# Kernel tuning notes

Measured on AMD Instinct MI355X. Metric: run time of the kernel, lower is better.

## Reference

```python
import jax, jax.numpy as jnp
import numpy as np

B, S, D = 2, 2048, 2048
H, G = 16, 4
HD = D // H          # head_dim = 128
KV = HD * G          # 512


def setup_inputs() -> dict:
    key = jax.random.key(0)
    ks = jax.random.split(key, 5)
    scale = 1.0 / np.sqrt(D)
    return {
        "x": jax.random.normal(ks[0], (B, S, D), dtype=jnp.float32),
        "Wqkv": jax.random.normal(ks[1], (D, D + 2 * KV), dtype=jnp.float32) * scale,
        "bqkv": jax.random.normal(ks[2], (D + 2 * KV,), dtype=jnp.float32) * 0.01,
        "Wout": jax.random.normal(ks[3], (D, D), dtype=jnp.float32) * scale,
        "bout": jax.random.normal(ks[4], (D,), dtype=jnp.float32) * 0.01,
    }


def reference(x, Wqkv, bqkv, Wout, bout):
    b, s, _ = x.shape
    qkv = x @ Wqkv + bqkv                                  # [b, s, D + 2*KV]
    q, k, v = jnp.split(qkv, [D, D + KV], axis=-1)
    q = q.reshape(b, s, H, HD)                             # [b, s, H, hd]
    # torch .repeat tiles the group axis: head h -> group (h % G)
    k = jnp.tile(k.reshape(b, s, G, HD), (1, 1, H // G, 1))  # [b, s, H, hd]
    v = jnp.tile(v.reshape(b, s, G, HD), (1, 1, H // G, 1))
    # NOTE: original divides by head_dim (not sqrt(head_dim)) -- kept faithfully
    scores = jnp.einsum("bqhd,bkhd->bhqk", q, k) / HD      # [b, H, s, s]
    prob = jax.nn.softmax(scores, axis=-1)
    out = jnp.einsum("bhqk,bkhd->bqhd", prob, v).reshape(b, s, D)
    return out @ Wout + bout
```

## Files before the change

### kernel.cpp

```cpp
#include <hip/hip_runtime.h>
#include <stdint.h>

typedef __bf16 bf16;
typedef __bf16 bf16x8 __attribute__((ext_vector_type(8)));
typedef __bf16 bf16x4 __attribute__((ext_vector_type(4)));
typedef float  f32x4  __attribute__((ext_vector_type(4)));

#define B_   2
#define S_   2048
#define D_   2048
#define H_   16
#define G_   4
#define HD_  128
#define KV_  512
#define NQKV 3072
#define M_   4096

__device__ __forceinline__ void async16(bf16* lds, const bf16* g) {
  __builtin_amdgcn_global_load_lds(
      (const __attribute__((address_space(1))) unsigned int*)g,
      (__attribute__((address_space(3))) unsigned int*)lds, 16, 0, 0);
}

__device__ __forceinline__ f32x4 mfma16(bf16x8 a, bf16x8 b, f32x4 c) {
  return __builtin_amdgcn_mfma_f32_16x16x32_bf16(a, b, c, 0, 0, 0);
}

__global__ void convert_x_kernel(const float* __restrict__ in,
                                 bf16* __restrict__ out, int n4) {
  int i = blockIdx.x * blockDim.x + threadIdx.x;
  if (i >= n4) return;
  float4 v = ((const float4*)in)[i];
  bf16x4 o = { (bf16)v.x, (bf16)v.y, (bf16)v.z, (bf16)v.w };
  *(bf16x4*)(out + (size_t)i * 4) = o;
}

__global__ void transpose_w_kernel(const float* __restrict__ in,
                                   bf16* __restrict__ out,
                                   int rows, int cols) {
  __shared__ float tile[32][33];
  int bc = blockIdx.x * 32;
  int br = blockIdx.y * 32;
  int tx = threadIdx.x, ty = threadIdx.y;
  #pragma unroll
  for (int i = 0; i < 32; i += 8)
    tile[ty + i][tx] = in[(size_t)(br + ty + i) * cols + bc + tx];
  __syncthreads();
  #pragma unroll
  for (int i = 0; i < 32; i += 8)
    out[(size_t)(bc + ty + i) * rows + br + tx] = (bf16)tile[tx][ty + i];
}

__global__ void transpose_v_kernel(const bf16* __restrict__ qkv,
                                   bf16* __restrict__ vt) {
  __shared__ bf16 tile[32][33];
  int bg = blockIdx.z; int b = bg / G_, g = bg % G_;
  int sb = blockIdx.x * 32, db = blockIdx.y * 32;
  int tx = threadIdx.x, ty = threadIdx.y;
  const bf16* src = qkv + (size_t)b * S_ * NQKV + (D_ + KV_ + g * HD_);
  #pragma unroll
  for (int i = 0; i < 32; i += 8)
    tile[ty + i][tx] = src[(size_t)(sb + ty + i) * NQKV + db + tx];
  __syncthreads();
  bf16* dst = vt + (size_t)(b * G_ + g) * HD_ * S_;
  #pragma unroll
  for (int i = 0; i < 32; i += 8)
    dst[(size_t)(db + ty + i) * S_ + sb + tx] = tile[tx][ty + i];
}

template <int OUT_BF16>
__global__ __launch_bounds__(256) void gemm_bt(const bf16* __restrict__ A,
                                               const bf16* __restrict__ Bt,
                                               const float* __restrict__ bias,
                                               void* __restrict__ Cout,
                                               int Ndim, int K) {
  __shared__ __align__(16) bf16 As[128 * 32];
  __shared__ __align__(16) bf16 Bs[128 * 32];
  int t = threadIdx.x;
  int w = t >> 6, l = t & 63, lr = l & 15, lg = l >> 4;
  int wm = w >> 1, wn = w & 1;
  int row0 = blockIdx.x * 128, col0 = blockIdx.y * 128;

  f32x4 acc[4][4] = {};

  const bf16* ga = A  + (size_t)(row0 + (t >> 2)) * K + (t & 3) * 8;
  const bf16* gb = Bt + (size_t)(col0 + (t >> 2)) * K + (t & 3) * 8;

  for (int k0 = 0; k0 < K; k0 += 32) {
    __syncthreads();
    #pragma unroll
    for (int i = 0; i < 2; i++)
      async16(&As[w * 512 + i * 2048], ga + (size_t)i * 64 * K + k0);
    #pragma unroll
    for (int i = 0; i < 2; i++)
      async16(&Bs[w * 512 + i * 2048], gb + (size_t)i * 64 * K + k0);
    __syncthreads();

    bf16x8 af[4], bfr[4];
    #pragma unroll
    for (int mi = 0; mi < 4; mi++)
      af[mi] = *(const bf16x8*)&As[(wm * 64 + mi * 16 + lr) * 32 + lg * 8];
    #pragma unroll
    for (int ni = 0; ni < 4; ni++)
      bfr[ni] = *(const bf16x8*)&Bs[(wn * 64 + ni * 16 + lr) * 32 + lg * 8];
    #pragma unroll
    for (int mi = 0; mi < 4; mi++)
      #pragma unroll
      for (int ni = 0; ni < 4; ni++)
        acc[mi][ni] = mfma16(af[mi], bfr[ni], acc[mi][ni]);
  }

  float bv[4];
  #pragma unroll
  for (int ni = 0; ni < 4; ni++)
    bv[ni] = bias[col0 + wn * 64 + ni * 16 + lr];

  #pragma unroll
  for (int mi = 0; mi < 4; mi++)
    #pragma unroll
    for (int ni = 0; ni < 4; ni++)
      #pragma unroll
      for (int r = 0; r < 4; r++) {
        int row = row0 + wm * 64 + mi * 16 + lg * 4 + r;
        int col = col0 + wn * 64 + ni * 16 + lr;
        float v = acc[mi][ni][r] + bv[ni];
        if (OUT_BF16)
          ((bf16*)Cout)[(size_t)row * Ndim + col] = (bf16)v;
        else
          ((float*)Cout)[(size_t)row * Ndim + col] = v;
      }
}

__global__ __launch_bounds__(256, 2) void attn_kernel(const bf16* __restrict__ qkv,
                                                      const bf16* __restrict__ vt,
                                                      bf16* __restrict__ attnb) {
  __shared__ __align__(16) bf16 Ks[64 * 128];
  __shared__ __align__(16) bf16 Vs[128 * 64];
  __shared__ __align__(16) bf16 Ps[4][32 * 64];

  int t = threadIdx.x, w = t >> 6, l = t & 63, lr = l & 15, lg = l >> 4;
  int rsw = lr & 7;
  int bh = blockIdx.y, b = bh >> 4, h = bh & 15, g = h & 3;
  int q0 = blockIdx.x * 128;

  bf16x8 qf[2][4];
  #pragma unroll
  for (int mi = 0; mi < 2; mi++) {
    const bf16* qbase = qkv + (size_t)(b * S_ + q0 + w * 32 + mi * 16 + lr) * NQKV + h * HD_;
    #pragma unroll
    for (int kc = 0; kc < 4; kc++)
      qf[mi][kc] = *(const bf16x8*)(qbase + kc * 32 + lg * 8);
  }

  const bf16* kbase = qkv + (size_t)b * S_ * NQKV + D_ + g * HD_;
  const bf16* vbase = vt + (size_t)(b * G_ + g) * HD_ * S_;

  int krowi = w * 4 + (l >> 4);
  int ksw = (l & 15) ^ (krowi & 7);
  const bf16* kgl = kbase + (size_t)krowi * NQKV + ksw * 8;
  int vrowi = w * 8 + (l >> 3);
  int vsw = (l & 7) ^ ((l >> 3) & 7);
  const bf16* vgl = vbase + (size_t)vrowi * S_ + vsw * 8;

  float lsum[2][4] = {};
  f32x4 accO[2][8] = {};

  for (int kv0 = 0; kv0 < S_; kv0 += 64) {
    __syncthreads();
    #pragma unroll
    for (int i = 0; i < 4; i++)
      async16(&Ks[w * 512 + i * 2048], kgl + (size_t)(kv0 + i * 16) * NQKV);
    #pragma unroll
    for (int i = 0; i < 4; i++)
      async16(&Vs[w * 512 + i * 2048], vgl + (size_t)(i * 32) * S_ + kv0);
    __syncthreads();

    f32x4 sacc[2][4] = {};
    __builtin_amdgcn_s_setprio(1);
    #pragma unroll
    for (int fk = 0; fk < 4; fk++) {
      bf16x8 kf[4];
      #pragma unroll
      for (int kc = 0; kc < 4; kc++)
        kf[kc] = *(const bf16x8*)&Ks[(fk * 16 + lr) * 128 + (((kc * 4 + lg) ^ rsw) * 8)];
      #pragma unroll
      for (int mi = 0; mi < 2; mi++)
        #pragma unroll
        for (int kc = 0; kc < 4; kc++)
          sacc[mi][fk] = mfma16(qf[mi][kc], kf[kc], sacc[mi][fk]);
    }
    __builtin_amdgcn_s_setprio(0);

    bf16* psw = &Ps[w][0];
    #pragma unroll
    for (int mi = 0; mi < 2; mi++)
      #pragma unroll
      for (int fk = 0; fk < 4; fk++)
        #pragma unroll
        for (int r = 0; r < 4; r++) {
          float pv = __expf(sacc[mi][fk][r] * 0.0078125f);
          lsum[mi][r] += pv;
          int prow = mi * 16 + lg * 4 + r;
          psw[prow * 64 + (((fk * 2 + (lr >> 3)) ^ (prow & 7)) * 8) + (lr & 7)] = (bf16)pv;
        }

    bf16x8 pa[2][2];
    #pragma unroll
    for (int mi = 0; mi < 2; mi++)
      #pragma unroll
      for (int kk = 0; kk < 2; kk++)
        pa[mi][kk] = *(const bf16x8*)&psw[(mi * 16 + lr) * 64 + (((kk * 4 + lg) ^ rsw) * 8)];

    __builtin_amdgcn_s_setprio(1);
    #pragma unroll
    for (int fd = 0; fd < 8; fd++) {
      bf16x8 vfr[2];
      #pragma unroll
      for (int kk = 0; kk < 2; kk++)
        vfr[kk] = *(const bf16x8*)&Vs[(fd * 16 + lr) * 64 + (((kk * 4 + lg) ^ rsw) * 8)];
      #pragma unroll
      for (int mi = 0; mi < 2; mi++)
        #pragma unroll
        for (int kk = 0; kk < 2; kk++)
          accO[mi][fd] = mfma16(pa[mi][kk], vfr[kk], accO[mi][fd]);
    }
    __builtin_amdgcn_s_setprio(0);
  }

  #pragma unroll
  for (int mi = 0; mi < 2; mi++)
    #pragma unroll
    for (int r = 0; r < 4; r++) {
      float s = lsum[mi][r];
      #pragma unroll
      for (int o = 1; o < 16; o <<= 1) s += __shfl_xor(s, o);
      lsum[mi][r] = 1.f / s;
    }

  #pragma unroll
  for (int mi = 0; mi < 2; mi++) {
    bf16* obase = attnb + (size_t)(b * S_ + q0 + w * 32 + mi * 16) * D_ + h * HD_;
    #pragma unroll
    for (int r = 0; r < 4; r++)
      #pragma unroll
      for (int fd = 0; fd < 8; fd++)
        obase[(size_t)(lg * 4 + r) * D_ + fd * 16 + lr] =
            (bf16)(accO[mi][fd][r] * lsum[mi][r]);
  }
}

extern "C" void kernel_launch(void* const* d_in, const int* in_sizes, int n_in,
                              void* d_out, int out_size, void* d_ws, size_t ws_size,
                              hipStream_t stream) {
  const float* x    = (const float*)d_in[0];
  const float* Wqkv = (const float*)d_in[1];
  const float* bqkv = (const float*)d_in[2];
  const float* Wout = (const float*)d_in[3];
  const float* bout = (const float*)d_in[4];
  float* out = (float*)d_out;

  char* p = (char*)d_ws;
  bf16* xb    = (bf16*)p; p += (size_t)M_ * D_ * 2;
  bf16* wqkvT = (bf16*)p; p += (size_t)NQKV * D_ * 2;
  bf16* woutT = (bf16*)p; p += (size_t)D_ * D_ * 2;
  bf16* qkvb  = (bf16*)p; p += (size_t)M_ * NQKV * 2;
  bf16* vtb   = (bf16*)p; p += (size_t)B_ * G_ * HD_ * S_ * 2;
  bf16* attnb = (bf16*)p; p += (size_t)M_ * D_ * 2;

  convert_x_kernel<<<dim3(M_ * D_ / 4 / 256), dim3(256), 0, stream>>>(x, xb, M_ * D_ / 4);
  transpose_w_kernel<<<dim3(NQKV / 32, D_ / 32), dim3(32, 8), 0, stream>>>(Wqkv, wqkvT, D_, NQKV);
  transpose_w_kernel<<<dim3(D_ / 32, D_ / 32), dim3(32, 8), 0, stream>>>(Wout, woutT, D_, D_);

  gemm_bt<1><<<dim3(M_ / 128, NQKV / 128), dim3(256), 0, stream>>>(xb, wqkvT, bqkv, (void*)qkvb, NQKV, D_);

  transpose_v_kernel<<<dim3(S_ / 32, HD_ / 32, B_ * G_), dim3(32, 8), 0, stream>>>(qkvb, vtb);

  attn_kernel<<<dim3(S_ / 128, B_ * H_), dim3(256), 0, stream>>>(qkvb, vtb, attnb);

  gemm_bt<0><<<dim3(M_ / 128, D_ / 128), dim3(256), 0, stream>>>(attnb, woutT, bout, (void*)out, D_, D_);
}
```

Before: 224.8 us.

## Pipeline GEMM with triple-buffered larger tiles and double-buffer attention KV loads

The bf16 GEMM now uses 512-thread blocks with 256x128 output tiles and a K-step of 64. It stages three LDS buffers with XOR-swizzled async loads, uses a counted vmcnt wait and a single barrier per step, and keeps two tiles in flight. The attention kernel double-buffers the K and V tiles so the next tile's global-to-LDS copy is issued before computing on the current one, which drops one barrier per iteration. The aim is to hide global memory latency behind MFMA work, at the cost of much more LDS per block (about 144KB in the GEMM, which limits it to one block per CU) and more attention LDS.

```diff
diff --git a/kernel.cpp b/kernel.cpp
--- a/kernel.cpp
+++ b/kernel.cpp
@@ -69,45 +69,82 @@
 }
 
 template <int OUT_BF16>
-__global__ __launch_bounds__(256) void gemm_bt(const bf16* __restrict__ A,
-                                               const bf16* __restrict__ Bt,
-                                               const float* __restrict__ bias,
-                                               void* __restrict__ Cout,
-                                               int Ndim, int K) {
-  __shared__ __align__(16) bf16 As[128 * 32];
-  __shared__ __align__(16) bf16 Bs[128 * 32];
+__global__ __launch_bounds__(512, 2) void gemm_bt(const bf16* __restrict__ A,
+                                                  const bf16* __restrict__ Bt,
+                                                  const float* __restrict__ bias,
+                                                  void* __restrict__ Cout,
+                                                  int Ndim, int K) {
+  __shared__ __align__(16) bf16 As[3][256 * 64];
+  __shared__ __align__(16) bf16 Bs[3][128 * 64];
+
   int t = threadIdx.x;
   int w = t >> 6, l = t & 63, lr = l & 15, lg = l >> 4;
   int wm = w >> 1, wn = w & 1;
-  int row0 = blockIdx.x * 128, col0 = blockIdx.y * 128;
+  int rsw = lr & 7;
+  int row0 = blockIdx.x * 256, col0 = blockIdx.y * 128;
+
+  int srow = t >> 3;
+  int schunk = (t & 7) ^ (srow & 7);
+  const bf16* ga = A  + (size_t)(row0 + srow) * K + schunk * 8;
+  const bf16* gb = Bt + (size_t)(col0 + srow) * K + schunk * 8;
+
+  const int NT = K >> 6;
+
+  auto STAGE = [&](int b, int kt) {
+    const bf16* a = ga + (size_t)kt * 64;
+    const bf16* bb = gb + (size_t)kt * 64;
+    #pragma unroll
+    for (int i = 0; i < 4; i++)
+      async16(&As[b][i * 4096 + w * 512], a + (size_t)i * 64 * K);
+    #pragma unroll
+    for (int i = 0; i < 2; i++)
+      async16(&Bs[b][i * 4096 + w * 512], bb + (size_t)i * 64 * K);
+  };
 
   f32x4 acc[4][4] = {};
 
-  const bf16* ga = A  + (size_t)(row0 + (t >> 2)) * K + (t & 3) * 8;
-  const bf16* gb = Bt + (size_t)(col0 + (t >> 2)) * K + (t & 3) * 8;
-
-  for (int k0 = 0; k0 < K; k0 += 32) {
-    __syncthreads();
-    #pragma unroll
-    for (int i = 0; i < 2; i++)
-      async16(&As[w * 512 + i * 2048], ga + (size_t)i * 64 * K + k0);
-    #pragma unroll
-    for (int i = 0; i < 2; i++)
-      async16(&Bs[w * 512 + i * 2048], gb + (size_t)i * 64 * K + k0);
-    __syncthreads();
-
-    bf16x8 af[4], bfr[4];
-    #pragma unroll
-    for (int mi = 0; mi < 4; mi++)
-      af[mi] = *(const bf16x8*)&As[(wm * 64 + mi * 16 + lr) * 32 + lg * 8];
+  STAGE(0, 0);
+  STAGE(1, 1);
+  int b0 = 0, b1 = 1, b2 = 2;
+
+  for (int kt = 0; kt < NT; ++kt) {
+    if (kt < NT - 1) {
+      asm volatile("s_waitcnt vmcnt(6)" ::: "memory");
+    } else {
+      asm volatile("s_waitcnt vmcnt(0)" ::: "memory");
+    }
+    __builtin_amdgcn_sched_barrier(0);
+    __builtin_amdgcn_s_barrier();
+    __builtin_amdgcn_sched_barrier(0);
+
+    if (kt + 2 < NT) STAGE(b2, kt + 2);
+
+    const bf16* as = &As[b0][0];
+    const bf16* bs = &Bs[b0][0];
+
+    bf16x8 bfr[4][2];
     #pragma unroll
     for (int ni = 0; ni < 4; ni++)
-      bfr[ni] = *(const bf16x8*)&Bs[(wn * 64 + ni * 16 + lr) * 32 + lg * 8];
-    #pragma unroll
-    for (int mi = 0; mi < 4; mi++)
-      #pragma unroll
-      for (int ni = 0; ni < 4; ni++)
-        acc[mi][ni] = mfma16(af[mi], bfr[ni], acc[mi][ni]);
+      #pragma unroll
+      for (int kk = 0; kk < 2; kk++)
+        bfr[ni][kk] = *(const bf16x8*)&bs[(wn * 64 + ni * 16 + lr) * 64 +
+                                          (((kk * 4 + lg) ^ rsw) * 8)];
+    __builtin_amdgcn_s_setprio(1);
+    #pragma unroll
+    for (int mi = 0; mi < 4; mi++) {
+      bf16x8 a0 = *(const bf16x8*)&as[(wm * 64 + mi * 16 + lr) * 64 +
+                                       (((0 + lg) ^ rsw) * 8)];
+      bf16x8 a1 = *(const bf16x8*)&as[(wm * 64 + mi * 16 + lr) * 64 +
+                                       (((4 + lg) ^ rsw) * 8)];
+      #pragma unroll
+      for (int ni = 0; ni < 4; ni++) {
+        acc[mi][ni] = mfma16(a0, bfr[ni][0], acc[mi][ni]);
+        acc[mi][ni] = mfma16(a1, bfr[ni][1], acc[mi][ni]);
+      }
+    }
+    __builtin_amdgcn_s_setprio(0);
+
+    int tmp = b0; b0 = b1; b1 = b2; b2 = tmp;
   }
 
   float bv[4];
@@ -134,8 +171,8 @@
 __global__ __launch_bounds__(256, 2) void attn_kernel(const bf16* __restrict__ qkv,
                                                       const bf16* __restrict__ vt,
                                                       bf16* __restrict__ attnb) {
-  __shared__ __align__(16) bf16 Ks[64 * 128];
-  __shared__ __align__(16) bf16 Vs[128 * 64];
+  __shared__ __align__(16) bf16 Ks[2][64 * 128];
+  __shared__ __align__(16) bf16 Vs[2][128 * 64];
   __shared__ __align__(16) bf16 Ps[4][32 * 64];
 
   int t = threadIdx.x, w = t >> 6, l = t & 63, lr = l & 15, lg = l >> 4;
@@ -162,19 +199,27 @@
   int vsw = (l & 7) ^ ((l >> 3) & 7);
   const bf16* vgl = vbase + (size_t)vrowi * S_ + vsw * 8;
 
+  auto STAGE_KV = [&](int nb, int kv0) {
+    #pragma unroll
+    for (int i = 0; i < 4; i++)
+      async16(&Ks[nb][w * 512 + i * 2048], kgl + (size_t)(kv0 + i * 16) * NQKV);
+    #pragma unroll
+    for (int i = 0; i < 4; i++)
+      async16(&Vs[nb][w * 512 + i * 2048], vgl + (size_t)(i * 32) * S_ + kv0);
+  };
+
   float lsum[2][4] = {};
   f32x4 accO[2][8] = {};
 
-  for (int kv0 = 0; kv0 < S_; kv0 += 64) {
+  STAGE_KV(0, 0);
+
+  for (int ti = 0; ti < S_ / 64; ++ti) {
+    int cur = ti & 1;
     __syncthreads();
-    #pragma unroll
-    for (int i = 0; i < 4; i++)
-      async16(&Ks[w * 512 + i * 2048], kgl + (size_t)(kv0 + i * 16) * NQKV);
-    #pragma unroll
-    for (int i = 0; i < 4; i++)
-      async16(&Vs[w * 512 + i * 2048], vgl + (size_t)(i * 32) * S_ + kv0);
-    __syncthreads();
-
+    if (ti + 1 < S_ / 64) STAGE_KV(cur ^ 1, (ti + 1) * 64);
+
+    const bf16* ks = &Ks[cur][0];
+    const bf16* vs = &Vs[cur][0];
     f32x4 sacc[2][4] = {};
     __builtin_amdgcn_s_setprio(1);
     #pragma unroll
@@ -182,7 +227,7 @@
       bf16x8 kf[4];
       #pragma unroll
       for (int kc = 0; kc < 4; kc++)
-        kf[kc] = *(const bf16x8*)&Ks[(fk * 16 + lr) * 128 + (((kc * 4 + lg) ^ rsw) * 8)];
+        kf[kc] = *(const bf16x8*)&ks[(fk * 16 + lr) * 128 + (((kc * 4 + lg) ^ rsw) * 8)];
       #pragma unroll
       for (int mi = 0; mi < 2; mi++)
         #pragma unroll
@@ -217,7 +262,7 @@
       bf16x8 vfr[2];
       #pragma unroll
       for (int kk = 0; kk < 2; kk++)
-        vfr[kk] = *(const bf16x8*)&Vs[(fd * 16 + lr) * 64 + (((kk * 4 + lg) ^ rsw) * 8)];
+        vfr[kk] = *(const bf16x8*)&vs[(fd * 16 + lr) * 64 + (((kk * 4 + lg) ^ rsw) * 8)];
       #pragma unroll
       for (int mi = 0; mi < 2; mi++)
         #pragma unroll
@@ -271,11 +316,11 @@
   transpose_w_kernel<<<dim3(NQKV / 32, D_ / 32), dim3(32, 8), 0, stream>>>(Wqkv, wqkvT, D_, NQKV);
   transpose_w_kernel<<<dim3(D_ / 32, D_ / 32), dim3(32, 8), 0, stream>>>(Wout, woutT, D_, D_);
 
-  gemm_bt<1><<<dim3(M_ / 128, NQKV / 128), dim3(256), 0, stream>>>(xb, wqkvT, bqkv, (void*)qkvb, NQKV, D_);
+  gemm_bt<1><<<dim3(M_ / 256, NQKV / 128), dim3(512), 0, stream>>>(xb, wqkvT, bqkv, (void*)qkvb, NQKV, D_);
 
   transpose_v_kernel<<<dim3(S_ / 32, HD_ / 32, B_ * G_), dim3(32, 8), 0, stream>>>(qkvb, vtb);
 
   attn_kernel<<<dim3(S_ / 128, B_ * H_), dim3(256), 0, stream>>>(qkvb, vtb, attnb);
 
-  gemm_bt<0><<<dim3(M_ / 128, D_ / 128), dim3(256), 0, stream>>>(attnb, woutT, bout, (void*)out, D_, D_);
-}
+  gemm_bt<0><<<dim3(M_ / 256, D_ / 128), dim3(512), 0, stream>>>(attnb, woutT, bout, (void*)out, D_, D_);
+}
```

Result: slower. 232.0 us (+3.2%).

## Double-buffer K/V tiles in attention, swizzle block order, transpose score MFMA

Applied to the files above, without the earlier changes.

The attention kernel now keeps two K/V shared-memory buffers. It issues the async loads for the next 64-key tile before computing on the current one, so global loads overlap with MFMA work and each iteration needs one barrier instead of two. Block indices are remapped so that neighbouring blocks cover different heads and batches, which is meant to change L2 locality. The score MFMA operands are swapped so each lane holds four consecutive keys for one query row. That allows packed 4-wide P stores and a row-sum reduction of two shuffles, finished through a small shared buffer. The cost is doubled K/V shared memory, which may limit occupancy.

```diff
diff --git a/kernel.cpp b/kernel.cpp
--- a/kernel.cpp
+++ b/kernel.cpp
@@ -134,14 +134,17 @@
 __global__ __launch_bounds__(256, 2) void attn_kernel(const bf16* __restrict__ qkv,
                                                       const bf16* __restrict__ vt,
                                                       bf16* __restrict__ attnb) {
-  __shared__ __align__(16) bf16 Ks[64 * 128];
-  __shared__ __align__(16) bf16 Vs[128 * 64];
+  __shared__ __align__(16) bf16 Ks[2][64 * 128];
+  __shared__ __align__(16) bf16 Vs[2][128 * 64];
   __shared__ __align__(16) bf16 Ps[4][32 * 64];
+  __shared__ float Ls[4][32];
 
   int t = threadIdx.x, w = t >> 6, l = t & 63, lr = l & 15, lg = l >> 4;
   int rsw = lr & 7;
-  int bh = blockIdx.y, b = bh >> 4, h = bh & 15, g = h & 3;
-  int q0 = blockIdx.x * 128;
+  int lin = blockIdx.x + gridDim.x * blockIdx.y;
+  int swz = (lin & 7) * 64 + (lin >> 3);
+  int q0 = (swz & 15) * 128;
+  int bh = swz >> 4, b = bh >> 4, h = bh & 15, g = h & 3;
 
   bf16x8 qf[2][4];
   #pragma unroll
@@ -162,18 +165,27 @@
   int vsw = (l & 7) ^ ((l >> 3) & 7);
   const bf16* vgl = vbase + (size_t)vrowi * S_ + vsw * 8;
 
-  float lsum[2][4] = {};
+  auto STAGE_KV = [&](int nb, int kv0) {
+    #pragma unroll
+    for (int i = 0; i < 4; i++)
+      async16(&Ks[nb][w * 512 + i * 2048], kgl + (size_t)(kv0 + i * 16) * NQKV);
+    #pragma unroll
+    for (int i = 0; i < 4; i++)
+      async16(&Vs[nb][w * 512 + i * 2048], vgl + (size_t)(i * 32) * S_ + kv0);
+  };
+
+  float lsump[2] = {};
   f32x4 accO[2][8] = {};
 
-  for (int kv0 = 0; kv0 < S_; kv0 += 64) {
+  STAGE_KV(0, 0);
+
+  for (int ti = 0; ti < S_ / 64; ++ti) {
+    int cur = ti & 1;
     __syncthreads();
-    #pragma unroll
-    for (int i = 0; i < 4; i++)
-      async16(&Ks[w * 512 + i * 2048], kgl + (size_t)(kv0 + i * 16) * NQKV);
-    #pragma unroll
-    for (int i = 0; i < 4; i++)
-      async16(&Vs[w * 512 + i * 2048], vgl + (size_t)(i * 32) * S_ + kv0);
-    __syncthreads();
+    if (ti + 1 < S_ / 64) STAGE_KV(cur ^ 1, (ti + 1) * 64);
+
+    const bf16* ks = &Ks[cur][0];
+    const bf16* vs = &Vs[cur][0];
 
     f32x4 sacc[2][4] = {};
     __builtin_amdgcn_s_setprio(1);
@@ -182,12 +194,12 @@
       bf16x8 kf[4];
       #pragma unroll
       for (int kc = 0; kc < 4; kc++)
-        kf[kc] = *(const bf16x8*)&Ks[(fk * 16 + lr) * 128 + (((kc * 4 + lg) ^ rsw) * 8)];
+        kf[kc] = *(const bf16x8*)&ks[(fk * 16 + lr) * 128 + (((kc * 4 + lg) ^ rsw) * 8)];
       #pragma unroll
       for (int mi = 0; mi < 2; mi++)
         #pragma unroll
         for (int kc = 0; kc < 4; kc++)
-          sacc[mi][fk] = mfma16(qf[mi][kc], kf[kc], sacc[mi][fk]);
+          sacc[mi][fk] = mfma16(kf[kc], qf[mi][kc], sacc[mi][fk]);
     }
     __builtin_amdgcn_s_setprio(0);
 
@@ -195,14 +207,16 @@
     #pragma unroll
     for (int mi = 0; mi < 2; mi++)
       #pragma unroll
-      for (int fk = 0; fk < 4; fk++)
-        #pragma unroll
-        for (int r = 0; r < 4; r++) {
-          float pv = __expf(sacc[mi][fk][r] * 0.0078125f);
-          lsum[mi][r] += pv;
-          int prow = mi * 16 + lg * 4 + r;
-          psw[prow * 64 + (((fk * 2 + (lr >> 3)) ^ (prow & 7)) * 8) + (lr & 7)] = (bf16)pv;
-        }
+      for (int fk = 0; fk < 4; fk++) {
+        float p0 = __expf(sacc[mi][fk][0] * 0.0078125f);
+        float p1 = __expf(sacc[mi][fk][1] * 0.0078125f);
+        float p2 = __expf(sacc[mi][fk][2] * 0.0078125f);
+        float p3 = __expf(sacc[mi][fk][3] * 0.0078125f);
+        lsump[mi] += (p0 + p1) + (p2 + p3);
+        bf16x4 pk = { (bf16)p0, (bf16)p1, (bf16)p2, (bf16)p3 };
+        *(bf16x4*)&psw[(mi * 16 + lr) * 64 +
+                       (((fk * 2 + (lg >> 1)) ^ rsw) * 8) + (lg & 1) * 4] = pk;
+      }
 
     bf16x8 pa[2][2];
     #pragma unroll
@@ -217,7 +231,7 @@
       bf16x8 vfr[2];
       #pragma unroll
       for (int kk = 0; kk < 2; kk++)
-        vfr[kk] = *(const bf16x8*)&Vs[(fd * 16 + lr) * 64 + (((kk * 4 + lg) ^ rsw) * 8)];
+        vfr[kk] = *(const bf16x8*)&vs[(fd * 16 + lr) * 64 + (((kk * 4 + lg) ^ rsw) * 8)];
       #pragma unroll
       for (int mi = 0; mi < 2; mi++)
         #pragma unroll
@@ -228,24 +242,25 @@
   }
 
   #pragma unroll
-  for (int mi = 0; mi < 2; mi++)
-    #pragma unroll
-    for (int r = 0; r < 4; r++) {
-      float s = lsum[mi][r];
-      #pragma unroll
-      for (int o = 1; o < 16; o <<= 1) s += __shfl_xor(s, o);
-      lsum[mi][r] = 1.f / s;
-    }
-
-  #pragma unroll
   for (int mi = 0; mi < 2; mi++) {
+    float s = lsump[mi];
+    s += __shfl_xor(s, 16);
+    s += __shfl_xor(s, 32);
+    if (lg == 0) Ls[w][mi * 16 + lr] = 1.f / s;
+  }
+
+  #pragma unroll
+  for (int mi = 0; mi < 2; mi++) {
+    float rls[4];
+    #pragma unroll
+    for (int r = 0; r < 4; r++) rls[r] = Ls[w][mi * 16 + lg * 4 + r];
     bf16* obase = attnb + (size_t)(b * S_ + q0 + w * 32 + mi * 16) * D_ + h * HD_;
     #pragma unroll
     for (int r = 0; r < 4; r++)
       #pragma unroll
       for (int fd = 0; fd < 8; fd++)
         obase[(size_t)(lg * 4 + r) * D_ + fd * 16 + lr] =
-            (bf16)(accO[mi][fd][r] * lsum[mi][r]);
+            (bf16)(accO[mi][fd][r] * rls[r]);
   }
 }
 
```

Result: slower. 259.2 us (+15.3%).
